# Kernel tuning notes

Hardware: AMD Instinct MI355X
Metric: run time of the kernel (lower is better)

The kernel has to match this reference:

```python
import jax, jax.numpy as jnp
import numpy as np

N = 65536   # total goals in library
D = 256     # flattened embedding dim
B = 2048    # batch_size (last B entries are the new batch)


def setup_inputs() -> dict:
    key = jax.random.key(0)
    k1, k2 = jax.random.split(key)
    return {
        "target_lib": jax.random.normal(k1, (N, D), dtype=jnp.float32),
        "reached_lib": jax.random.normal(k2, (N, D), dtype=jnp.float32),
        "batch_size": B,
    }


def _euclid(a, b):
    # distance_fn: Euclidean distance between two embeddings
    return jnp.sqrt(jnp.sum((a - b) ** 2))


def _nearest_idx(queries, lib):
    # top-1 nearest neighbor via squared-distance expansion (same argmin as cdist)
    qn = jnp.sum(queries * queries, axis=1, keepdims=True)      # [B,1]
    ln = jnp.sum(lib * lib, axis=1)                             # [L]
    d2 = qn + ln[None, :] - 2.0 * (queries @ lib.T)             # [B,L]
    return jnp.argmin(d2, axis=1)                               # [B]


def reference(target_lib, reached_lib, batch_size):
    targets = target_lib[-batch_size:]          # [B,D] newest target goals
    reached = reached_lib[-batch_size:]         # [B,D] newest reached goals
    prev = reached_lib[:-batch_size]            # [N-B,D] previously reached goals

    prev_closest = prev[_nearest_idx(targets, prev)]       # [B,D]
    new_closest = reached[_nearest_idx(targets, reached)]  # [B,D]

    def LP(t, init_e, reached_e):
        return _euclid(t, init_e) - _euclid(t, reached_e)

    IM_vals, IM_grads = jax.vmap(jax.value_and_grad(LP, 0))(
        targets, prev_closest, new_closest)
    return IM_vals, IM_grads
```

## Files before the change

kernel.cpp:

```cpp
#include <hip/hip_runtime.h>
#include <math.h>

#define NTOT   65536
#define DDIM   256
#define BATCH  2048
#define NPREV  (NTOT - BATCH)

#define NC_P 16
#define CHUNK_P 3968
#define NC_R 8
#define CHUNK_R 256

#define INF_F 3.402823466e+38f
#define SWZ(r) ((((r) & 3)) ^ ((((r) >> 2) & 3)))

typedef float  f32x4  __attribute__((ext_vector_type(4)));
typedef float  f32x16 __attribute__((ext_vector_type(16)));
typedef _Float16 half8 __attribute__((ext_vector_type(8)));

#define TILE_HALVES 65536
#define KB_HALVES   8192

#define SCHED_FENCE() __builtin_amdgcn_sched_barrier(0)
#define RAW_BARRIER() do { SCHED_FENCE(); __builtin_amdgcn_s_barrier(); SCHED_FENCE(); } while (0)
#define VMCNT2()  do { asm volatile("s_waitcnt vmcnt(2)" ::: "memory"); SCHED_FENCE(); } while (0)
#define VMCNT0()  do { asm volatile("s_waitcnt vmcnt(0)" ::: "memory"); SCHED_FENCE(); } while (0)

__global__ void lp_norms(const float* __restrict__ lib, float* __restrict__ ln) {
    const int row  = blockIdx.x * 4 + (threadIdx.x >> 6);
    const int lane = threadIdx.x & 63;
    const float4 v = reinterpret_cast<const float4*>(lib + (size_t)row * DDIM)[lane];
    float s = v.x * v.x + v.y * v.y + v.z * v.z + v.w * v.w;
#pragma unroll
    for (int off = 32; off > 0; off >>= 1) s += __shfl_down(s, off);
    if (lane == 0) ln[row] = s;
}

__device__ __forceinline__ void cvt_split(const f32x4 a, const f32x4 b,
                                          half8& h, half8& l) {
    float v[8] = {a[0], a[1], a[2], a[3], b[0], b[1], b[2], b[3]};
#pragma unroll
    for (int j = 0; j < 8; ++j) {
        const float s = v[j] * 256.0f;
        const _Float16 hh = (_Float16)s;
        const _Float16 ll = (_Float16)(s - (float)hh);
        h[j] = hh; l[j] = ll;
    }
}

__global__ void lp_split32(const float* __restrict__ src, _Float16* __restrict__ dst,
                           float* __restrict__ ln) {
    const int tile = blockIdx.x;
    const int t    = threadIdx.x;
    const int rg   = t >> 6;
    const int l    = t & 63;
    const int row  = rg * 32 + (l & 31);
    const int k8   = l >> 5;
    const float* srcR = src + (size_t)tile * 128 * DDIM + (size_t)row * DDIM;
    _Float16*    dstT = dst + (size_t)tile * TILE_HALVES;

    float nsum = 0.f;
#pragma unroll
    for (int kb = 0; kb < 8; ++kb) {
#pragma unroll
        for (int kk = 0; kk < 2; ++kk) {
            const float* p = srcR + kb * 32 + kk * 16 + k8 * 8;
            const f32x4 a = *reinterpret_cast<const f32x4*>(p);
            const f32x4 b = *reinterpret_cast<const f32x4*>(p + 4);
            half8 h, lo; cvt_split(a, b, h, lo);
            const size_t off = ((size_t)(((kb * 2 + 0) * 4 + rg) * 2 + kk) * 64 + l) * 8;
            *reinterpret_cast<half8*>(dstT + off)        = h;
            *reinterpret_cast<half8*>(dstT + off + 4096) = lo;
            nsum += a[0]*a[0] + a[1]*a[1] + a[2]*a[2] + a[3]*a[3]
                  + b[0]*b[0] + b[1]*b[1] + b[2]*b[2] + b[3]*b[3];
        }
    }
    nsum += __shfl_xor(nsum, 32);
    if (ln != nullptr && k8 == 0) ln[(size_t)tile * 128 + row] = nsum;
}

__device__ __forceinline__ void stage8(_Float16* lds, const _Float16* g, int t) {
    __builtin_amdgcn_global_load_lds(
        (const __attribute__((address_space(1))) void*)(g + (size_t)t * 8),
        (__attribute__((address_space(3))) void*)(lds + (size_t)(t >> 6) * 512),
        16, 0, 0);
}

__global__ __launch_bounds__(512, 1)
void lp_nn_mfma7(const _Float16* __restrict__ Qs, const _Float16* __restrict__ Ls,
                 const float* __restrict__ ln, int chunkRows,
                 float* __restrict__ pscore, int* __restrict__ pidx, int nchunks)
{
    __shared__ _Float16 QB[65536];
    __shared__ _Float16 LB[2][8192];

    const int nwg  = 16 * nchunks;
    const int hid  = blockIdx.x;
    const int work = (hid & 7) * (nwg >> 3) + (hid >> 3);
    const int bx   = work & 15;
    const int by   = work >> 4;

    const int t    = threadIdx.x;
    const int lane = t & 63;
    const int wid  = t >> 6;
    const int wq   = wid >> 1;
    const int wl   = wid & 1;
    const int col  = lane & 31, hi = lane >> 5;
    const int chunkBase = by * chunkRows;
    const int NT   = chunkRows >> 7;

    const _Float16* Qt    = Qs + (size_t)bx * TILE_HALVES;
    const _Float16* Lbase = Ls + (size_t)(chunkBase >> 7) * TILE_HALVES;

    float bkey[16];
    int   bidx[16];
    f32x16 acc[2];
#pragma unroll
    for (int r = 0; r < 16; ++r) { bkey[r] = INF_F; bidx[r] = 0x7fffffff; }
    acc[0] = (f32x16)(0.f); acc[1] = (f32x16)(0.f);

    auto stageL = [&](_Float16* dst, int lt, int kb) {
        const _Float16* src = Lbase + (size_t)lt * TILE_HALVES + kb * KB_HALVES;
        stage8(dst,        src,        t);
        stage8(dst + 4096, src + 4096, t);
    };

#pragma unroll
    for (int i = 0; i < 16; ++i) stage8(QB + i * 4096, Qt + i * 4096, t);
    stageL(LB[0], 0, 0);
    stageL(LB[1], 0, 1);

    float lnv0 = 0.f, lnv1 = 0.f;

    for (int lt = 0; lt < NT; ++lt) {
#pragma unroll
        for (int kb = 0; kb < 8; ++kb) {
            if (lt == NT - 1 && kb == 7) VMCNT0(); else VMCNT2();
            RAW_BARRIER();
            if (kb == 0) {
                lnv0 = ln[chunkBase + lt * 128 + wl * 64 + col];
                lnv1 = ln[chunkBase + lt * 128 + wl * 64 + 32 + col];
            }
            half8 av[2][2];
#pragma unroll
            for (int hl = 0; hl < 2; ++hl)
#pragma unroll
                for (int kk = 0; kk < 2; ++kk)
                    av[hl][kk] = *reinterpret_cast<const half8*>(
                        QB + kb * 8192 + hl * 4096 + wq * 1024 + kk * 512 + lane * 8);
            half8 bv[2][2][2];
#pragma unroll
            for (int nf = 0; nf < 2; ++nf)
#pragma unroll
                for (int hl = 0; hl < 2; ++hl)
#pragma unroll
                    for (int kk = 0; kk < 2; ++kk)
                        bv[nf][hl][kk] = *reinterpret_cast<const half8*>(
                            LB[kb & 1] + hl * 4096 + (wl * 2 + nf) * 1024 + kk * 512 + lane * 8);
            __builtin_amdgcn_s_setprio(1);
#pragma unroll
            for (int nf = 0; nf < 2; ++nf)
#pragma unroll
                for (int kk = 0; kk < 2; ++kk) {
                    acc[nf] = __builtin_amdgcn_mfma_f32_32x32x16_f16(av[0][kk], bv[nf][0][kk], acc[nf], 0, 0, 0);
                    acc[nf] = __builtin_amdgcn_mfma_f32_32x32x16_f16(av[0][kk], bv[nf][1][kk], acc[nf], 0, 0, 0);
                    acc[nf] = __builtin_amdgcn_mfma_f32_32x32x16_f16(av[1][kk], bv[nf][0][kk], acc[nf], 0, 0, 0);
                }
            __builtin_amdgcn_s_setprio(0);
            RAW_BARRIER();
            {
                const int s2lt = lt + ((kb + 2) >> 3);
                const int s2kb = (kb + 2) & 7;
                if (s2lt < NT) stageL(LB[kb & 1], s2lt, s2kb);
            }
            if (kb == 7) {
#pragma unroll
                for (int nf = 0; nf < 2; ++nf) {
                    const int gidx = chunkBase + lt * 128 + wl * 64 + nf * 32 + col;
                    const float lnvs = (nf ? lnv1 : lnv0) * 65536.0f;
#pragma unroll
                    for (int r = 0; r < 16; ++r) {
                        const float key = fmaf(-2.f, acc[nf][r], lnvs);
                        if (key < bkey[r] || (key == bkey[r] && gidx < bidx[r])) {
                            bkey[r] = key; bidx[r] = gidx;
                        }
                        acc[nf][r] = 0.f;
                    }
                }
            }
        }
    }

#pragma unroll
    for (int off = 1; off < 32; off <<= 1)
#pragma unroll
        for (int r = 0; r < 16; ++r) {
            const float ok = __shfl_xor(bkey[r], off);
            const int   oi = __shfl_xor(bidx[r], off);
            if (ok < bkey[r] || (ok == bkey[r] && oi < bidx[r])) {
                bkey[r] = ok; bidx[r] = oi;
            }
        }

    float* xk = (float*)&LB[0][0];
    int*   xi = (int*)  &LB[0][1024];
    if (col == 0)
#pragma unroll
        for (int r = 0; r < 16; ++r) {
            const int q = wq * 32 + (r & 3) + 8 * (r >> 2) + 4 * hi;
            xk[wl * 128 + q] = bkey[r];
            xi[wl * 128 + q] = bidx[r];
        }
    __syncthreads();
    if (t < 128) {
        float bk = xk[t]; int bi = xi[t];
        const float k2 = xk[128 + t]; const int i2 = xi[128 + t];
        if (k2 < bk || (k2 == bk && i2 < bi)) { bk = k2; bi = i2; }
        const int q = bx * 128 + t;
        pscore[(size_t)q * nchunks + by] = bk;
        pidx  [(size_t)q * nchunks + by] = bi;
    }
}

__global__ __launch_bounds__(256, 2)
void lp_nn_mfma_fb(const float* __restrict__ Q, const float* __restrict__ L,
                   const float* __restrict__ ln, int chunkRows,
                   float* __restrict__ pscore, int* __restrict__ pidx, int nchunks)
{
    __shared__ _Float16 Ah[128 * 32];
    __shared__ _Float16 Al[128 * 32];
    __shared__ _Float16 Bh[128 * 32];
    __shared__ _Float16 Bl[128 * 32];
    __shared__ float xk[2][128];
    __shared__ int   xi[2][128];

    const int t    = threadIdx.x;
    const int wid  = t >> 6, lane = t & 63;
    const int wq   = wid >> 1, wl = wid & 1;
    const int col  = lane & 15, rg = lane >> 4;
    const int qbase = blockIdx.x * 128;
    const int chunkBase = blockIdx.y * chunkRows;
    const int srow   = t >> 2;
    const int schunk = t & 3;

    float bkey[4][4];
    int   bidxr[4][4];
#pragma unroll
    for (int mf = 0; mf < 4; ++mf)
#pragma unroll
        for (int i = 0; i < 4; ++i) { bkey[mf][i] = INF_F; bidxr[mf][i] = 0x7fffffff; }

    for (int lt = 0; lt < chunkRows; lt += 128) {
        f32x4 acc[4][4];
#pragma unroll
        for (int mf = 0; mf < 4; ++mf)
#pragma unroll
            for (int nf = 0; nf < 4; ++nf) acc[mf][nf] = (f32x4)(0.f);

        for (int kb = 0; kb < DDIM; kb += 32) {
            __syncthreads();
#pragma unroll
            for (int sr = 0; sr < 2; ++sr) {
                const int r = srow + 64 * sr;
                const int s = schunk ^ SWZ(r);
                {
                    const float* src = Q + (size_t)(qbase + r) * DDIM + kb + schunk * 8;
                    const f32x4 a = *reinterpret_cast<const f32x4*>(src);
                    const f32x4 b = *reinterpret_cast<const f32x4*>(src + 4);
                    half8 h, l; cvt_split(a, b, h, l);
                    *reinterpret_cast<half8*>(&Ah[r * 32 + s * 8]) = h;
                    *reinterpret_cast<half8*>(&Al[r * 32 + s * 8]) = l;
                }
                {
                    const float* src = L + (size_t)(chunkBase + lt + r) * DDIM + kb + schunk * 8;
                    const f32x4 a = *reinterpret_cast<const f32x4*>(src);
                    const f32x4 b = *reinterpret_cast<const f32x4*>(src + 4);
                    half8 h, l; cvt_split(a, b, h, l);
                    *reinterpret_cast<half8*>(&Bh[r * 32 + s * 8]) = h;
                    *reinterpret_cast<half8*>(&Bl[r * 32 + s * 8]) = l;
                }
            }
            __syncthreads();

            half8 ah[4], al[4];
#pragma unroll
            for (int mf = 0; mf < 4; ++mf) {
                const int r = wq * 64 + mf * 16 + col;
                const int s = rg ^ SWZ(r);
                ah[mf] = *reinterpret_cast<const half8*>(&Ah[r * 32 + s * 8]);
                al[mf] = *reinterpret_cast<const half8*>(&Al[r * 32 + s * 8]);
            }
#pragma unroll
            for (int nf = 0; nf < 4; ++nf) {
                const int r = wl * 64 + nf * 16 + col;
                const int s = rg ^ SWZ(r);
                const half8 bh = *reinterpret_cast<const half8*>(&Bh[r * 32 + s * 8]);
                const half8 bl = *reinterpret_cast<const half8*>(&Bl[r * 32 + s * 8]);
#pragma unroll
                for (int mf = 0; mf < 4; ++mf) {
                    acc[mf][nf] = __builtin_amdgcn_mfma_f32_16x16x32_f16(ah[mf], bh, acc[mf][nf], 0, 0, 0);
                    acc[mf][nf] = __builtin_amdgcn_mfma_f32_16x16x32_f16(ah[mf], bl, acc[mf][nf], 0, 0, 0);
                    acc[mf][nf] = __builtin_amdgcn_mfma_f32_16x16x32_f16(al[mf], bh, acc[mf][nf], 0, 0, 0);
                }
            }
        }

#pragma unroll
        for (int nf = 0; nf < 4; ++nf) {
            const int gidx = chunkBase + lt + wl * 64 + nf * 16 + col;
            const float lnv = ln[gidx] * 65536.0f;
#pragma unroll
            for (int mf = 0; mf < 4; ++mf)
#pragma unroll
                for (int i = 0; i < 4; ++i) {
                    const float key = fmaf(-2.f, acc[mf][nf][i], lnv);
                    if (key < bkey[mf][i] || (key == bkey[mf][i] && gidx < bidxr[mf][i])) {
                        bkey[mf][i] = key; bidxr[mf][i] = gidx;
                    }
                }
        }
    }

#pragma unroll
    for (int off = 1; off < 16; off <<= 1)
#pragma unroll
        for (int mf = 0; mf < 4; ++mf)
#pragma unroll
            for (int i = 0; i < 4; ++i) {
                const float ok = __shfl_xor(bkey[mf][i], off);
                const int   oi = __shfl_xor(bidxr[mf][i], off);
                if (ok < bkey[mf][i] || (ok == bkey[mf][i] && oi < bidxr[mf][i])) {
                    bkey[mf][i] = ok; bidxr[mf][i] = oi;
                }
            }
    if (col == 0)
#pragma unroll
        for (int mf = 0; mf < 4; ++mf)
#pragma unroll
            for (int i = 0; i < 4; ++i) {
                const int ql = wq * 64 + mf * 16 + rg * 4 + i;
                xk[wl][ql] = bkey[mf][i];
                xi[wl][ql] = bidxr[mf][i];
            }
    __syncthreads();
    if (t < 128) {
        float bk = xk[0][t]; int bi = xi[0][t];
        const float k2 = xk[1][t]; const int i2 = xi[1][t];
        if (k2 < bk || (k2 == bk && i2 < bi)) { bk = k2; bi = i2; }
        const int q = qbase + t;
        pscore[(size_t)q * nchunks + blockIdx.y] = bk;
        pidx  [(size_t)q * nchunks + blockIdx.y] = bi;
    }
}

__global__ void lp_finalize(const float* __restrict__ Q,
                            const float* __restrict__ prevL,
                            const float* __restrict__ reachL,
                            const float* __restrict__ ps_p, const int* __restrict__ pi_p,
                            const float* __restrict__ ps_r, const int* __restrict__ pi_r,
                            float* __restrict__ out)
{
    const int q = blockIdx.x;
    const int lane = threadIdx.x;

    float k1 = (lane < NC_P) ? ps_p[(size_t)q * NC_P + lane] : INF_F;
    int   i1 = (lane < NC_P) ? pi_p[(size_t)q * NC_P + lane] : 0x7fffffff;
#pragma unroll
    for (int off = 32; off > 0; off >>= 1) {
        const float ok = __shfl_xor(k1, off);
        const int   oi = __shfl_xor(i1, off);
        if (ok < k1 || (ok == k1 && oi < i1)) { k1 = ok; i1 = oi; }
    }
    float k2 = (lane < NC_R) ? ps_r[(size_t)q * NC_R + lane] : INF_F;
    int   i2 = (lane < NC_R) ? pi_r[(size_t)q * NC_R + lane] : 0x7fffffff;
#pragma unroll
    for (int off = 32; off > 0; off >>= 1) {
        const float ok = __shfl_xor(k2, off);
        const int   oi = __shfl_xor(i2, off);
        if (ok < k2 || (ok == k2 && oi < i2)) { k2 = ok; i2 = oi; }
    }

    const float4 tv = reinterpret_cast<const float4*>(Q      + (size_t)q  * DDIM)[lane];
    const float4 e1 = reinterpret_cast<const float4*>(prevL  + (size_t)i1 * DDIM)[lane];
    const float4 e2 = reinterpret_cast<const float4*>(reachL + (size_t)i2 * DDIM)[lane];
    const float4 d1 = {tv.x - e1.x, tv.y - e1.y, tv.z - e1.z, tv.w - e1.w};
    const float4 d2 = {tv.x - e2.x, tv.y - e2.y, tv.z - e2.z, tv.w - e2.w};
    float s1 = d1.x * d1.x + d1.y * d1.y + d1.z * d1.z + d1.w * d1.w;
    float s2 = d2.x * d2.x + d2.y * d2.y + d2.z * d2.z + d2.w * d2.w;
#pragma unroll
    for (int off = 32; off > 0; off >>= 1) {
        s1 += __shfl_xor(s1, off);
        s2 += __shfl_xor(s2, off);
    }
    const float r1 = sqrtf(s1), r2 = sqrtf(s2);
    float4 g;
    g.x = d1.x / r1 - d2.x / r2;
    g.y = d1.y / r1 - d2.y / r2;
    g.z = d1.z / r1 - d2.z / r2;
    g.w = d1.w / r1 - d2.w / r2;
    reinterpret_cast<float4*>(out + BATCH + (size_t)q * DDIM)[lane] = g;
    if (lane == 0) out[q] = r1 - r2;
}

extern "C" void kernel_launch(void* const* d_in, const int* in_sizes, int n_in,
                              void* d_out, int out_size, void* d_ws, size_t ws_size,
                              hipStream_t stream) {
    const float* target_lib  = (const float*)d_in[0];
    const float* reached_lib = (const float*)d_in[1];
    const float* Qp     = target_lib  + (size_t)NPREV * DDIM;
    const float* prevL  = reached_lib;
    const float* reachL = reached_lib + (size_t)NPREV * DDIM;

    float* ws     = (float*)d_ws;
    float* ln_all = ws;
    float* ps_p   = ln_all + NTOT;
    float* ps_r   = ps_p + (size_t)BATCH * NC_P;
    int*   pi_p   = (int*)(ps_r + (size_t)BATCH * NC_R);
    int*   pi_r   = pi_p + (size_t)BATCH * NC_P;
    _Float16* Qsp = (_Float16*)(pi_r + (size_t)BATCH * NC_R);
    _Float16* Lsp = Qsp + (size_t)(BATCH / 128) * TILE_HALVES;
    float* out    = (float*)d_out;

    const size_t need = (size_t)(NTOT + 2 * BATCH * (NC_P + NC_R)) * 4
                      + (size_t)(BATCH / 128 + NTOT / 128) * TILE_HALVES * 2;

    if (ws_size >= need) {
        lp_split32<<<NTOT / 128, 256, 0, stream>>>(reached_lib, Lsp, ln_all);
        lp_split32<<<BATCH / 128, 256, 0, stream>>>(Qp, Qsp, nullptr);
        lp_nn_mfma7<<<16 * NC_P, 512, 0, stream>>>(
            Qsp, Lsp, ln_all, CHUNK_P, ps_p, pi_p, NC_P);
        lp_nn_mfma7<<<16 * NC_R, 512, 0, stream>>>(
            Qsp, Lsp + (size_t)(NPREV / 128) * TILE_HALVES,
            ln_all + NPREV, CHUNK_R, ps_r, pi_r, NC_R);
    } else {
        lp_norms<<<NTOT / 4, 256, 0, stream>>>(reached_lib, ln_all);
        lp_nn_mfma_fb<<<dim3(BATCH / 128, 31), 256, 0, stream>>>(
            Qp, prevL, ln_all, 2048, ps_p, pi_p, 31);
        lp_nn_mfma_fb<<<dim3(BATCH / 128, 16), 256, 0, stream>>>(
            Qp, reachL, ln_all + NPREV, 128, ps_r, pi_r, 16);
    }
    lp_finalize<<<BATCH, 64, 0, stream>>>(Qp, prevL, reachL, ps_p, pi_p, ps_r, pi_r, out);
}
```

Measured before the change: 254.6 us.

## Switch NN kernel to 256-thread blocks with 2x2 MFMA register tiles per wave

The nearest-neighbour MFMA kernel drops from 512 to 256 threads per block. Each wave now computes a 2x2 grid of 32x32 fragments, so every fragment loaded from LDS feeds more MFMAs. The prev and reached searches are rebalanced to 16 chunks each, using 31 tiles per chunk for prev and 1 tile for reached, with matching changes to the load-wait count and the finalize arguments. Register pressure rises because the per-row best-key and index arrays double, and the reached pass does very little work per block.

```diff
diff --git a/kernel.cpp b/kernel.cpp
--- a/kernel.cpp
+++ b/kernel.cpp
@@ -6,10 +6,11 @@
 #define BATCH  2048
 #define NPREV  (NTOT - BATCH)
 
-#define NC_P 16
-#define CHUNK_P 3968
-#define NC_R 8
-#define CHUNK_R 256
+#define FNC    16
+#define TPC_P  31
+#define TPC_R  1
+#define BNC_P  31
+#define BNC_R  16
 
 #define INF_F 3.402823466e+38f
 #define SWZ(r) ((((r) & 3)) ^ ((((r) >> 2) & 3)))
@@ -23,7 +24,7 @@
 
 #define SCHED_FENCE() __builtin_amdgcn_sched_barrier(0)
 #define RAW_BARRIER() do { SCHED_FENCE(); __builtin_amdgcn_s_barrier(); SCHED_FENCE(); } while (0)
-#define VMCNT2()  do { asm volatile("s_waitcnt vmcnt(2)" ::: "memory"); SCHED_FENCE(); } while (0)
+#define VMCNT4()  do { asm volatile("s_waitcnt vmcnt(4)" ::: "memory"); SCHED_FENCE(); } while (0)
 #define VMCNT0()  do { asm volatile("s_waitcnt vmcnt(0)" ::: "memory"); SCHED_FENCE(); } while (0)
 
 __global__ void lp_norms(const float* __restrict__ lib, float* __restrict__ ln) {
@@ -79,19 +80,18 @@
     if (ln != nullptr && k8 == 0) ln[(size_t)tile * 128 + row] = nsum;
 }
 
-__device__ __forceinline__ void stage8(_Float16* lds, const _Float16* g, int t) {
+__device__ __forceinline__ void gload16(const _Float16* g, _Float16* lds) {
     __builtin_amdgcn_global_load_lds(
-        (const __attribute__((address_space(1))) void*)(g + (size_t)t * 8),
-        (__attribute__((address_space(3))) void*)(lds + (size_t)(t >> 6) * 512),
-        16, 0, 0);
-}
-
-__global__ __launch_bounds__(512, 1)
-void lp_nn_mfma7(const _Float16* __restrict__ Qs, const _Float16* __restrict__ Ls,
-                 const float* __restrict__ ln, int chunkRows,
-                 float* __restrict__ pscore, int* __restrict__ pidx, int nchunks)
+        (const __attribute__((address_space(1))) void*)g,
+        (__attribute__((address_space(3))) void*)lds, 16, 0, 0);
+}
+
+__global__ __launch_bounds__(256, 1)
+void lp_nn_mfma8(const _Float16* __restrict__ Qs, const _Float16* __restrict__ Ls,
+                 const float* __restrict__ ln, int tilesPC, int nchunks,
+                 float* __restrict__ pscore, int* __restrict__ pidx)
 {
-    __shared__ _Float16 QB[65536];
+    __shared__ _Float16 QB[TILE_HALVES];
     __shared__ _Float16 LB[2][8192];
 
     const int nwg  = 16 * nchunks;
@@ -106,87 +106,97 @@
     const int wq   = wid >> 1;
     const int wl   = wid & 1;
     const int col  = lane & 31, hi = lane >> 5;
-    const int chunkBase = by * chunkRows;
-    const int NT   = chunkRows >> 7;
+
+    const int tb      = by * tilesPC;
+    const int rowBase = tb * 128;
+    const int NT      = tilesPC;
+    const int NSTEP   = NT * 8;
 
     const _Float16* Qt    = Qs + (size_t)bx * TILE_HALVES;
-    const _Float16* Lbase = Ls + (size_t)(chunkBase >> 7) * TILE_HALVES;
-
-    float bkey[16];
-    int   bidx[16];
-    f32x16 acc[2];
-#pragma unroll
-    for (int r = 0; r < 16; ++r) { bkey[r] = INF_F; bidx[r] = 0x7fffffff; }
-    acc[0] = (f32x16)(0.f); acc[1] = (f32x16)(0.f);
-
-    auto stageL = [&](_Float16* dst, int lt, int kb) {
-        const _Float16* src = Lbase + (size_t)lt * TILE_HALVES + kb * KB_HALVES;
-        stage8(dst,        src,        t);
-        stage8(dst + 4096, src + 4096, t);
+    const _Float16* Lbase = Ls + (size_t)tb * TILE_HALVES;
+
+    float bkey[2][16];
+    int   bidxr[2][16];
+    f32x16 acc[2][2];
+#pragma unroll
+    for (int mf = 0; mf < 2; ++mf) {
+#pragma unroll
+        for (int r = 0; r < 16; ++r) { bkey[mf][r] = INF_F; bidxr[mf][r] = 0x7fffffff; }
+#pragma unroll
+        for (int nf = 0; nf < 2; ++nf) acc[mf][nf] = (f32x16)(0.f);
+    }
+
+    auto stage4 = [&](_Float16* dst, const _Float16* src) {
+        gload16(src + t * 8, dst + (size_t)(t >> 6) * 512);
     };
-
-#pragma unroll
-    for (int i = 0; i < 16; ++i) stage8(QB + i * 4096, Qt + i * 4096, t);
-    stageL(LB[0], 0, 0);
-    stageL(LB[1], 0, 1);
+    auto stageL = [&](int s) {
+        const _Float16* base = Lbase + (size_t)(s >> 3) * TILE_HALVES + (s & 7) * KB_HALVES;
+        _Float16* dst = LB[s & 1];
+#pragma unroll
+        for (int i = 0; i < 4; ++i) stage4(dst + i * 2048, base + i * 2048);
+    };
+
+#pragma unroll
+    for (int i = 0; i < 32; ++i) stage4(QB + i * 2048, Qt + i * 2048);
+    stageL(0);
+    stageL(1);
 
     float lnv0 = 0.f, lnv1 = 0.f;
 
-    for (int lt = 0; lt < NT; ++lt) {
-#pragma unroll
-        for (int kb = 0; kb < 8; ++kb) {
-            if (lt == NT - 1 && kb == 7) VMCNT0(); else VMCNT2();
-            RAW_BARRIER();
-            if (kb == 0) {
-                lnv0 = ln[chunkBase + lt * 128 + wl * 64 + col];
-                lnv1 = ln[chunkBase + lt * 128 + wl * 64 + 32 + col];
-            }
-            half8 av[2][2];
+    for (int s = 0; s < NSTEP; ++s) {
+        const int lt = s >> 3, kb = s & 7;
+        if (s == NSTEP - 1) VMCNT0(); else VMCNT4();
+        RAW_BARRIER();
+        if (kb == 0) {
+            lnv0 = ln[rowBase + lt * 128 + wl * 64 + col];
+            lnv1 = ln[rowBase + lt * 128 + wl * 64 + 32 + col];
+        }
+        const _Float16* Ab = QB + kb * KB_HALVES;
+        const _Float16* Bb = LB[s & 1];
+        half8 a[2][2][2], b[2][2][2];
+#pragma unroll
+        for (int mf = 0; mf < 2; ++mf)
 #pragma unroll
             for (int hl = 0; hl < 2; ++hl)
 #pragma unroll
-                for (int kk = 0; kk < 2; ++kk)
-                    av[hl][kk] = *reinterpret_cast<const half8*>(
-                        QB + kb * 8192 + hl * 4096 + wq * 1024 + kk * 512 + lane * 8);
-            half8 bv[2][2][2];
-#pragma unroll
-            for (int nf = 0; nf < 2; ++nf)
-#pragma unroll
-                for (int hl = 0; hl < 2; ++hl)
-#pragma unroll
-                    for (int kk = 0; kk < 2; ++kk)
-                        bv[nf][hl][kk] = *reinterpret_cast<const half8*>(
-                            LB[kb & 1] + hl * 4096 + (wl * 2 + nf) * 1024 + kk * 512 + lane * 8);
-            __builtin_amdgcn_s_setprio(1);
-#pragma unroll
-            for (int nf = 0; nf < 2; ++nf)
-#pragma unroll
                 for (int kk = 0; kk < 2; ++kk) {
-                    acc[nf] = __builtin_amdgcn_mfma_f32_32x32x16_f16(av[0][kk], bv[nf][0][kk], acc[nf], 0, 0, 0);
-                    acc[nf] = __builtin_amdgcn_mfma_f32_32x32x16_f16(av[0][kk], bv[nf][1][kk], acc[nf], 0, 0, 0);
-                    acc[nf] = __builtin_amdgcn_mfma_f32_32x32x16_f16(av[1][kk], bv[nf][0][kk], acc[nf], 0, 0, 0);
-                }
-            __builtin_amdgcn_s_setprio(0);
-            RAW_BARRIER();
-            {
-                const int s2lt = lt + ((kb + 2) >> 3);
-                const int s2kb = (kb + 2) & 7;
-                if (s2lt < NT) stageL(LB[kb & 1], s2lt, s2kb);
-            }
-            if (kb == 7) {
-#pragma unroll
-                for (int nf = 0; nf < 2; ++nf) {
-                    const int gidx = chunkBase + lt * 128 + wl * 64 + nf * 32 + col;
-                    const float lnvs = (nf ? lnv1 : lnv0) * 65536.0f;
+                    a[mf][hl][kk] = *reinterpret_cast<const half8*>(
+                        Ab + hl * 4096 + (wq * 2 + mf) * 1024 + kk * 512 + lane * 8);
+                    b[mf][hl][kk] = *reinterpret_cast<const half8*>(
+                        Bb + hl * 4096 + (wl * 2 + mf) * 1024 + kk * 512 + lane * 8);
+                }
+        __builtin_amdgcn_s_setprio(1);
+#pragma unroll
+        for (int kk = 0; kk < 2; ++kk)
+#pragma unroll
+            for (int term = 0; term < 3; ++term) {
+                const int ta = (term == 2) ? 1 : 0;
+                const int tb2 = (term == 1) ? 1 : 0;
+#pragma unroll
+                for (int mf = 0; mf < 2; ++mf)
+#pragma unroll
+                    for (int nf = 0; nf < 2; ++nf)
+                        acc[mf][nf] = __builtin_amdgcn_mfma_f32_32x32x16_f16(
+                            a[mf][ta][kk], b[nf][tb2][kk], acc[mf][nf], 0, 0, 0);
+            }
+        __builtin_amdgcn_s_setprio(0);
+        RAW_BARRIER();
+        if (s + 2 < NSTEP) stageL(s + 2);
+        if (kb == 7) {
+#pragma unroll
+            for (int nf = 0; nf < 2; ++nf) {
+                const int gidx = rowBase + lt * 128 + wl * 64 + nf * 32 + col;
+                const float lnvs = (nf ? lnv1 : lnv0) * 65536.0f;
+#pragma unroll
+                for (int mf = 0; mf < 2; ++mf)
 #pragma unroll
                     for (int r = 0; r < 16; ++r) {
-                        const float key = fmaf(-2.f, acc[nf][r], lnvs);
-                        if (key < bkey[r] || (key == bkey[r] && gidx < bidx[r])) {
-                            bkey[r] = key; bidx[r] = gidx;
+                        const float key = fmaf(-2.f, acc[mf][nf][r], lnvs);
+                        if (key < bkey[mf][r] || (key == bkey[mf][r] && gidx < bidxr[mf][r])) {
+                            bkey[mf][r] = key; bidxr[mf][r] = gidx;
                         }
-                        acc[nf][r] = 0.f;
+                        acc[mf][nf][r] = 0.f;
                     }
-                }
             }
         }
     }
@@ -194,23 +204,28 @@
 #pragma unroll
     for (int off = 1; off < 32; off <<= 1)
 #pragma unroll
-        for (int r = 0; r < 16; ++r) {
-            const float ok = __shfl_xor(bkey[r], off);
-            const int   oi = __shfl_xor(bidx[r], off);
-            if (ok < bkey[r] || (ok == bkey[r] && oi < bidx[r])) {
-                bkey[r] = ok; bidx[r] = oi;
-            }
-        }
+        for (int mf = 0; mf < 2; ++mf)
+#pragma unroll
+            for (int r = 0; r < 16; ++r) {
+                const float ok = __shfl_xor(bkey[mf][r], off);
+                const int   oi = __shfl_xor(bidxr[mf][r], off);
+                if (ok < bkey[mf][r] || (ok == bkey[mf][r] && oi < bidxr[mf][r])) {
+                    bkey[mf][r] = ok; bidxr[mf][r] = oi;
+                }
+            }
 
     float* xk = (float*)&LB[0][0];
     int*   xi = (int*)  &LB[0][1024];
+    RAW_BARRIER();
     if (col == 0)
 #pragma unroll
-        for (int r = 0; r < 16; ++r) {
-            const int q = wq * 32 + (r & 3) + 8 * (r >> 2) + 4 * hi;
-            xk[wl * 128 + q] = bkey[r];
-            xi[wl * 128 + q] = bidx[r];
-        }
+        for (int mf = 0; mf < 2; ++mf)
+#pragma unroll
+            for (int r = 0; r < 16; ++r) {
+                const int q = wq * 64 + mf * 32 + (r & 3) + 8 * (r >> 2) + 4 * hi;
+                xk[wl * 128 + q] = bkey[mf][r];
+                xi[wl * 128 + q] = bidxr[mf][r];
+            }
     __syncthreads();
     if (t < 128) {
         float bk = xk[t]; int bi = xi[t];
@@ -358,21 +373,22 @@
                             const float* __restrict__ reachL,
                             const float* __restrict__ ps_p, const int* __restrict__ pi_p,
                             const float* __restrict__ ps_r, const int* __restrict__ pi_r,
+                            int ncp, int ncr,
                             float* __restrict__ out)
 {
     const int q = blockIdx.x;
     const int lane = threadIdx.x;
 
-    float k1 = (lane < NC_P) ? ps_p[(size_t)q * NC_P + lane] : INF_F;
-    int   i1 = (lane < NC_P) ? pi_p[(size_t)q * NC_P + lane] : 0x7fffffff;
+    float k1 = (lane < ncp) ? ps_p[(size_t)q * ncp + lane] : INF_F;
+    int   i1 = (lane < ncp) ? pi_p[(size_t)q * ncp + lane] : 0x7fffffff;
 #pragma unroll
     for (int off = 32; off > 0; off >>= 1) {
         const float ok = __shfl_xor(k1, off);
         const int   oi = __shfl_xor(i1, off);
         if (ok < k1 || (ok == k1 && oi < i1)) { k1 = ok; i1 = oi; }
     }
-    float k2 = (lane < NC_R) ? ps_r[(size_t)q * NC_R + lane] : INF_F;
-    int   i2 = (lane < NC_R) ? pi_r[(size_t)q * NC_R + lane] : 0x7fffffff;
+    float k2 = (lane < ncr) ? ps_r[(size_t)q * ncr + lane] : INF_F;
+    int   i2 = (lane < ncr) ? pi_r[(size_t)q * ncr + lane] : 0x7fffffff;
 #pragma unroll
     for (int off = 32; off > 0; off >>= 1) {
         const float ok = __shfl_xor(k2, off);
@@ -414,30 +430,33 @@
     float* ws     = (float*)d_ws;
     float* ln_all = ws;
     float* ps_p   = ln_all + NTOT;
-    float* ps_r   = ps_p + (size_t)BATCH * NC_P;
-    int*   pi_p   = (int*)(ps_r + (size_t)BATCH * NC_R);
-    int*   pi_r   = pi_p + (size_t)BATCH * NC_P;
-    _Float16* Qsp = (_Float16*)(pi_r + (size_t)BATCH * NC_R);
+    float* ps_r   = ps_p + (size_t)BATCH * BNC_P;
+    int*   pi_p   = (int*)(ps_r + (size_t)BATCH * BNC_R);
+    int*   pi_r   = pi_p + (size_t)BATCH * BNC_P;
+    _Float16* Qsp = (_Float16*)(pi_r + (size_t)BATCH * BNC_R);
     _Float16* Lsp = Qsp + (size_t)(BATCH / 128) * TILE_HALVES;
     float* out    = (float*)d_out;
 
-    const size_t need = (size_t)(NTOT + 2 * BATCH * (NC_P + NC_R)) * 4
+    const size_t need = (size_t)(NTOT + 2 * BATCH * (BNC_P + BNC_R)) * 4
                       + (size_t)(BATCH / 128 + NTOT / 128) * TILE_HALVES * 2;
 
     if (ws_size >= need) {
         lp_split32<<<NTOT / 128, 256, 0, stream>>>(reached_lib, Lsp, ln_all);
         lp_split32<<<BATCH / 128, 256, 0, stream>>>(Qp, Qsp, nullptr);
-        lp_nn_mfma7<<<16 * NC_P, 512, 0, stream>>>(
-            Qsp, Lsp, ln_all, CHUNK_P, ps_p, pi_p, NC_P);
-        lp_nn_mfma7<<<16 * NC_R, 512, 0, stream>>>(
+        lp_nn_mfma8<<<16 * FNC, 256, 0, stream>>>(
+            Qsp, Lsp, ln_all, TPC_P, FNC, ps_p, pi_p);
+        lp_nn_mfma8<<<16 * FNC, 256, 0, stream>>>(
             Qsp, Lsp + (size_t)(NPREV / 128) * TILE_HALVES,
-            ln_all + NPREV, CHUNK_R, ps_r, pi_r, NC_R);
+            ln_all + NPREV, TPC_R, FNC, ps_r, pi_r);
+        lp_finalize<<<BATCH, 64, 0, stream>>>(
+            Qp, prevL, reachL, ps_p, pi_p, ps_r, pi_r, FNC, FNC, out);
     } else {
         lp_norms<<<NTOT / 4, 256, 0, stream>>>(reached_lib, ln_all);
-        lp_nn_mfma_fb<<<dim3(BATCH / 128, 31), 256, 0, stream>>>(
-            Qp, prevL, ln_all, 2048, ps_p, pi_p, 31);
-        lp_nn_mfma_fb<<<dim3(BATCH / 128, 16), 256, 0, stream>>>(
-            Qp, reachL, ln_all + NPREV, 128, ps_r, pi_r, 16);
-    }
-    lp_finalize<<<BATCH, 64, 0, stream>>>(Qp, prevL, reachL, ps_p, pi_p, ps_r, pi_r, out);
-}
+        lp_nn_mfma_fb<<<dim3(BATCH / 128, BNC_P), 256, 0, stream>>>(
+            Qp, prevL, ln_all, 2048, ps_p, pi_p, BNC_P);
+        lp_nn_mfma_fb<<<dim3(BATCH / 128, BNC_R), 256, 0, stream>>>(
+            Qp, reachL, ln_all + NPREV, 128, ps_r, pi_r, BNC_R);
+        lp_finalize<<<BATCH, 64, 0, stream>>>(
+            Qp, prevL, reachL, ps_p, pi_p, ps_r, pi_r, BNC_P, BNC_R, out);
+    }
+}
```

Result: slower. 414.3 us (+62.8%).
